# Optimization experiments

Measured on AMD Instinct MI355X. Metric: run time of the kernel, lower is better.

The kernel has to match this reference:

```python
import jax, jax.numpy as jnp
import numpy as np
import math

E = 8192        # number of hyperedges in the batch
IN_DIM = 256
OUT_DIM = 128


def setup_inputs() -> dict:
    key = jax.random.key(0)
    k1, k2, k3, k4 = jax.random.split(key, 4)
    node_embeddings = jax.random.normal(k1, (E, IN_DIM), dtype=jnp.float32)
    # xavier_uniform-like scale for the projection weights
    lim = 1.414 * math.sqrt(6.0 / (IN_DIM + OUT_DIM))
    query_weight = jax.random.uniform(k2, (IN_DIM, OUT_DIM), minval=-lim, maxval=lim, dtype=jnp.float32)
    key_weight = jax.random.uniform(k3, (IN_DIM, OUT_DIM), minval=-lim, maxval=lim, dtype=jnp.float32)
    # binary hypergraph connectivity mask [E, E]; diagonal forced to 1 so no row is fully masked
    mask = jax.random.randint(k4, (E, E), 0, 2, dtype=jnp.int32)
    mask = mask.at[jnp.arange(E), jnp.arange(E)].set(1)
    return {
        "node_embeddings": node_embeddings,
        "query_weight": query_weight,
        "key_weight": key_weight,
        "attention_mask": mask,
    }


def reference(node_embeddings, query_weight, key_weight, attention_mask):
    # QK projections: [E, in] x [in, out] -> [E, out]
    q = node_embeddings @ query_weight
    k = node_embeddings @ key_weight
    # scaled scores [E, E]
    scores = (q @ k.T) / jnp.sqrt(jnp.asarray(OUT_DIM, dtype=q.dtype))
    # masked_fill(mask == 0, -inf)
    scores = jnp.where(attention_mask == 0, jnp.asarray(-jnp.inf, dtype=scores.dtype), scores)
    probs = jax.nn.softmax(scores, axis=1)
    # output aggregates the KEY projections (as in the original code)
    return probs @ k
```

## Files before the change

### kernel.cpp

```cpp
#include <hip/hip_runtime.h>
#include <stdint.h>

#define E_N 8192
#define SPLIT 8
#define CH 16
#define QBLK 64

typedef unsigned short u16;
typedef unsigned int u32;
typedef unsigned long long u64;
typedef __attribute__((ext_vector_type(4))) float f32x4;
typedef __attribute__((ext_vector_type(8))) short bf16x8;
typedef __attribute__((ext_vector_type(4))) unsigned int u32x4;
typedef __attribute__((ext_vector_type(2))) unsigned int u32x2;

union V16 { u32x4 q; bf16x8 h; u16 u[8]; };

static __device__ __forceinline__ u16 f2bf(float f) {
  union { float f; unsigned u; } c; c.f = f;
  unsigned r = c.u + 0x7FFFu + ((c.u >> 16) & 1u);
  return (u16)(r >> 16);
}

constexpr float QS = 1.4426950408889634f / 11.313708498984761f;

__global__ void k_wt(const float* __restrict__ Wq, const float* __restrict__ Wk,
                     u16* __restrict__ wt) {
  int idx = blockIdx.x * 256 + threadIdx.x;
  int mat = idx >> 15, rem = idx & 32767;
  float v = mat ? Wk[rem] : Wq[rem];
  int d = rem >> 7, c = rem & 127;
  wt[(mat * 128 + c) * 256 + d] = f2bf(v);
}

__launch_bounds__(256)
__global__ void k_proj(const float* __restrict__ X, const u16* __restrict__ wt,
                       u16* __restrict__ qg, u16* __restrict__ kg) {
  __shared__ __align__(16) char Xs[64 * 512];
  const int tid = threadIdx.x;
  const int wid = tid >> 6, lane = tid & 63, g = lane >> 4, l15 = lane & 15;
  const int r0 = blockIdx.x * 64;
#pragma unroll
  for (int i = 0; i < 16; ++i) {
    int s = tid + 256 * i;
    int row = s >> 6, c4 = (s & 63) << 2;
    f32x4 v = *(const f32x4*)(X + (size_t)(r0 + row) * 256 + c4);
    u32x2 pk;
    pk[0] = f2bf(v[0]) | ((unsigned)f2bf(v[1]) << 16);
    pk[1] = f2bf(v[2]) | ((unsigned)f2bf(v[3]) << 16);
    *(u32x2*)(Xs + (((row << 9) + (c4 << 1)) ^ ((row & 7) << 4))) = pk;
  }
  __syncthreads();
  bf16x8 xa[8];
  const int arow = wid * 16 + l15;
#pragma unroll
  for (int ks = 0; ks < 8; ++ks) {
    V16 t; t.q = *(const u32x4*)(Xs + (((arow << 9) + (ks << 6) + (g << 4)) ^ ((l15 & 7) << 4)));
    xa[ks] = t.h;
  }
  const f32x4 zero4 = {0.f, 0.f, 0.f, 0.f};
  f32x4 acc[16];
#pragma unroll
  for (int i = 0; i < 16; ++i) acc[i] = zero4;
#pragma unroll
  for (int ct = 0; ct < 16; ++ct) {
    int mat = ct >> 3, c = ((ct & 7) << 4) + l15;
#pragma unroll
    for (int ks = 0; ks < 8; ++ks) {
      V16 b; b.q = *(const u32x4*)(wt + ((mat * 128 + c) * 256 + (ks << 5) + (g << 3)));
      acc[ct] = __builtin_amdgcn_mfma_f32_16x16x32_bf16(xa[ks], b.h, acc[ct], 0, 0, 0);
    }
  }
#pragma unroll
  for (int ct = 0; ct < 16; ++ct) {
    int mat = ct >> 3, c = ((ct & 7) << 4) + l15;
#pragma unroll
    for (int r = 0; r < 4; ++r) {
      int row = r0 + wid * 16 + 4 * g + r;
      float v = acc[ct][r];
      if (mat == 0) qg[row * 128 + c] = f2bf(v * QS);
      else          kg[row * 128 + c] = f2bf(v);
    }
  }
}

__global__ void k_kt(const u16* __restrict__ kg, u16* __restrict__ ktg) {
  __shared__ __align__(16) u16 Ts[64 * 66];
  const int tid = threadIdx.x;
  const int b = blockIdx.x;
  const int r0 = (b >> 1) * 64, c0 = (b & 1) * 64;
#pragma unroll
  for (int i = 0; i < 2; ++i) {
    int s = tid + 256 * i;
    int row = s >> 3, seg = s & 7;
    u32x4 v = *(const u32x4*)(kg + (size_t)(r0 + row) * 128 + c0 + seg * 8);
    unsigned* dst = (unsigned*)((char*)Ts + row * 132 + seg * 16);
    dst[0] = v[0]; dst[1] = v[1]; dst[2] = v[2]; dst[3] = v[3];
  }
  __syncthreads();
#pragma unroll
  for (int i = 0; i < 2; ++i) {
    int s = tid + 256 * i;
    int oc = s >> 3, seg2 = s & 7;
    u16 t[8];
#pragma unroll
    for (int j = 0; j < 8; ++j) t[j] = Ts[(seg2 * 8 + j) * 66 + oc];
    u32x4 o;
    o[0] = t[0] | ((unsigned)t[1] << 16);
    o[1] = t[2] | ((unsigned)t[3] << 16);
    o[2] = t[4] | ((unsigned)t[5] << 16);
    o[3] = t[6] | ((unsigned)t[7] << 16);
    *(u32x4*)(ktg + (size_t)(c0 + oc) * E_N + r0 + seg2 * 8) = o;
  }
}

#define LOADREGS(KV1)                                                           \
  {                                                                             \
    const u16* kp = kgp + (size_t)(KV1) * 128;                                  \
    kr0 = *(const u32x4*)(kp);                                                  \
    kr1 = *(const u32x4*)(kp + 16 * 128);                                       \
    kr2 = *(const u32x4*)(kp + 32 * 128);                                       \
    kr3 = *(const u32x4*)(kp + 48 * 128);                                       \
    const u16* tp = ktp + (KV1);                                                \
    tr0 = *(const u32x4*)(tp);                                                  \
    tr1 = *(const u32x4*)(tp + 32 * E_N);                                       \
    tr2 = *(const u32x4*)(tp + 64 * E_N);                                       \
    tr3 = *(const u32x4*)(tp + 96 * E_N);                                       \
  }

#define WRITELDS(KW, TW)                                                        \
  {                                                                             \
    *(u32x4*)((KW) + kofs)          = kr0;                                      \
    *(u32x4*)((KW) + kofs + 4096)   = kr1;                                      \
    *(u32x4*)((KW) + kofs + 8192)   = kr2;                                      \
    *(u32x4*)((KW) + kofs + 12288)  = kr3;                                      \
    *(u32x4*)((TW) + tofs)          = tr0;                                      \
    *(u32x4*)((TW) + tofs + 4096)   = tr1;                                      \
    *(u32x4*)((TW) + tofs + 8192)   = tr2;                                      \
    *(u32x4*)((TW) + tofs + 12288)  = tr3;                                      \
  }

#define MASKLOAD(KV1)                                                           \
  {                                                                             \
    _Pragma("unroll")                                                           \
    for (int j = 0; j < 16; ++j) mv[j] = mptr[(size_t)j * E_N + (KV1)];         \
  }

#define MASKBALLOT()                                                            \
  {                                                                             \
    u32 mlo = 0, mhi = 0;                                                       \
    _Pragma("unroll")                                                           \
    for (int j = 0; j < 16; ++j) {                                              \
      u64 b = __ballot(mv[j] != 0);                                             \
      if (lane == j) { mlo = (u32)b; mhi = (u32)(b >> 32); }                    \
    }                                                                           \
    if (lane < 16) { u32x2 o; o[0] = mlo; o[1] = mhi;                           \
      *(u32x2*)(MshW + lane * 2) = o; }                                         \
  }

#define FSTEP(SUB, KR, TR, KW, TW, DOPF)                                        \
  {                                                                             \
    if (DOPF) {                                                                 \
      LOADREGS(kvbase + (st2 + (SUB) + 1) * 64)                                 \
      MASKLOAD(kvbase + (st2 + (SUB) + 1) * 64)                                 \
    }                                                                           \
    u32 wlo[4], whi[4];                                                         \
    _Pragma("unroll")                                                           \
    for (int r = 0; r < 4; ++r) {                                               \
      u32x2 t3 = *(const u32x2*)(MshW + (4 * g + r) * 2);                       \
      wlo[r] = t3[0]; whi[r] = t3[1];                                           \
    }                                                                           \
    f32x4 S[4];                                                                 \
    _Pragma("unroll")                                                           \
    for (int t = 0; t < 4; ++t) S[t] = zero4;                                   \
    _Pragma("unroll")                                                           \
    for (int t = 0; t < 4; ++t) {                                               \
      int krow = t * 16 + l15;                                                  \
      _Pragma("unroll")                                                         \
      for (int ks = 0; ks < 4; ++ks) {                                          \
        V16 kf; kf.q = *(const u32x4*)((KR) + (((krow << 8) + (ks << 6) + (g << 4)) ^ ((l15 & 7) << 4))); \
        S[t] = __builtin_amdgcn_mfma_f32_16x16x32_bf16(qf[ks], kf.h, S[t], 0, 0, 0); \
      }                                                                         \
    }                                                                           \
    _Pragma("unroll")                                                           \
    for (int t = 0; t < 4; ++t) {                                               \
      _Pragma("unroll")                                                         \
      for (int r = 0; r < 4; ++r) {                                             \
        u32 w = (t & 2) ? whi[r] : wlo[r];                                      \
        float pv = ((w >> ((t & 1) * 16 + l15)) & 1u)                           \
                       ? __builtin_amdgcn_exp2f(S[t][r]) : 0.f;                 \
        lacc[r] += pv;                                                          \
        int prow = 4 * g + r;                                                   \
        *(u16*)(Pw + ((prow * 128 + (t * 16 + l15) * 2) ^ ((prow & 7) << 4))) = f2bf(pv); \
      }                                                                         \
    }                                                                           \
    bf16x8 pa0, pa1;                                                            \
    { V16 t2; t2.q = *(const u32x4*)(Pw + ((l15 * 128 + g * 16) ^ ((l15 & 7) << 4))); pa0 = t2.h; } \
    { V16 t2; t2.q = *(const u32x4*)(Pw + ((l15 * 128 + 64 + g * 16) ^ ((l15 & 7) << 4))); pa1 = t2.h; } \
    _Pragma("unroll")                                                           \
    for (int dt = 0; dt < 8; ++dt) {                                            \
      int krow = dt * 16 + l15;                                                 \
      V16 kf0; kf0.q = *(const u32x4*)((TR) + (((krow << 7) + (g << 4)) ^ ((l15 & 7) << 4))); \
      Oacc[dt] = __builtin_amdgcn_mfma_f32_16x16x32_bf16(pa0, kf0.h, Oacc[dt], 0, 0, 0); \
      V16 kf1; kf1.q = *(const u32x4*)((TR) + (((krow << 7) + 64 + (g << 4)) ^ ((l15 & 7) << 4))); \
      Oacc[dt] = __builtin_amdgcn_mfma_f32_16x16x32_bf16(pa1, kf1.h, Oacc[dt], 0, 0, 0); \
    }                                                                           \
    if (DOPF) MASKBALLOT()                                                      \
    __syncthreads();                                                            \
    if (DOPF) WRITELDS(KW, TW)                                                  \
    __syncthreads();                                                            \
  }

__launch_bounds__(256, 2)
__global__ void k_flash(const u16* __restrict__ qg, const u16* __restrict__ kg,
                        const u16* __restrict__ ktg, const int* __restrict__ M,
                        float* __restrict__ Op, float* __restrict__ lp) {
  __shared__ __align__(16) char K0[64 * 256], K1[64 * 256];
  __shared__ __align__(16) char T0[128 * 128], T1[128 * 128];
  __shared__ __align__(16) char Psh[4 * 2048];
  __shared__ __align__(8)  u32 Msh[4 * 32];
  const int tid = threadIdx.x;
  const int wid = tid >> 6, lane = tid & 63, g = lane >> 4, l15 = lane & 15;
  const int bid = blockIdx.x;
  const int split = bid & 7, qb = bid >> 3;
  const int qb0 = qb * QBLK;
  const int kvbase = split * (E_N / SPLIT);
  char* Pw = Psh + wid * 2048;
  u32* MshW = Msh + wid * 32;
  const int* mptr = M + (size_t)(qb0 + wid * 16) * E_N + lane;
  int mv[16];

  const int kr_r = tid >> 4, kr_s = tid & 15;
  const int tr_d = tid >> 3, tr_s = tid & 7;
  const int kofs = ((kr_r << 8) + (kr_s << 4)) ^ ((kr_r & 7) << 4);
  const int tofs = ((tr_d << 7) + (tr_s << 4)) ^ ((tr_d & 7) << 4);
  const u16* kgp = kg + (size_t)kr_r * 128 + kr_s * 8;
  const u16* ktp = ktg + (size_t)tr_d * E_N + tr_s * 8;
  u32x4 kr0, kr1, kr2, kr3, tr0, tr1, tr2, tr3;

  bf16x8 qf[4];
  {
    const u16* qrow = qg + (size_t)(qb0 + wid * 16 + l15) * 128;
#pragma unroll
    for (int ks = 0; ks < 4; ++ks) {
      V16 t; t.q = *(const u32x4*)(qrow + (ks << 5) + (g << 3));
      qf[ks] = t.h;
    }
  }
  const f32x4 zero4 = {0.f, 0.f, 0.f, 0.f};
  f32x4 Oacc[8];
#pragma unroll
  for (int i = 0; i < 8; ++i) Oacc[i] = zero4;
  float lacc[4] = {0.f, 0.f, 0.f, 0.f};

  MASKLOAD(kvbase)
  MASKBALLOT()
  LOADREGS(kvbase)
  WRITELDS(K0, T0)
  __syncthreads();

  for (int st2 = 0; st2 < CH; st2 += 2) {
    FSTEP(0, K0, T0, K1, T1, true)
    FSTEP(1, K1, T1, K0, T0, (st2 < CH - 2))
  }

#pragma unroll
  for (int r = 0; r < 4; ++r) {
    float v = lacc[r];
    v += __shfl_xor(v, 1);
    v += __shfl_xor(v, 2);
    v += __shfl_xor(v, 4);
    v += __shfl_xor(v, 8);
    lacc[r] = v;
  }
  if (l15 == 0) {
#pragma unroll
    for (int r = 0; r < 4; ++r)
      lp[split * E_N + qb0 + wid * 16 + 4 * g + r] = lacc[r];
  }
  float* op = Op + ((size_t)split * E_N + qb0 + wid * 16) * 128;
#pragma unroll
  for (int dt = 0; dt < 8; ++dt)
#pragma unroll
    for (int r = 0; r < 4; ++r)
      op[(4 * g + r) * 128 + dt * 16 + l15] = Oacc[dt][r];
}

__global__ void k_comb(const float* __restrict__ Op, const float* __restrict__ lp,
                       float* __restrict__ out) {
  int idx4 = blockIdx.x * 256 + threadIdx.x;
  int base = idx4 << 2;
  int e = base >> 7;
  f32x4 o = {0.f, 0.f, 0.f, 0.f};
  float l = 0.f;
#pragma unroll
  for (int s = 0; s < SPLIT; ++s) {
    o += *(const f32x4*)(Op + (size_t)s * (E_N * 128) + base);
    l += lp[s * E_N + e];
  }
  float rl = 1.0f / l;
  o[0] *= rl; o[1] *= rl; o[2] *= rl; o[3] *= rl;
  *(f32x4*)(out + base) = o;
}

extern "C" void kernel_launch(void* const* d_in, const int* in_sizes, int n_in,
                              void* d_out, int out_size, void* d_ws, size_t ws_size,
                              hipStream_t stream) {
  const float* X  = (const float*)d_in[0];
  const float* Wq = (const float*)d_in[1];
  const float* Wk = (const float*)d_in[2];
  const int*   M  = (const int*)d_in[3];
  char* ws = (char*)d_ws;
  u16*   qg   = (u16*)(ws);
  u16*   kg   = (u16*)(ws + (size_t)(2u << 20));
  u16*   ktg  = (u16*)(ws + (size_t)(4u << 20));
  u16*   wt   = (u16*)(ws + (size_t)(6u << 20));
  float* lp   = (float*)(ws + (size_t)(6u << 20) + (128u << 10));
  float* Op   = (float*)(ws + (size_t)(6u << 20) + (512u << 10) + (8u << 20));
  float* out = (float*)d_out;

  k_wt  <<<256, 256, 0, stream>>>(Wq, Wk, wt);
  k_proj<<<128, 256, 0, stream>>>(X, wt, qg, kg);
  k_kt  <<<256, 256, 0, stream>>>(kg, ktg);
  k_flash<<<SPLIT * (E_N / QBLK), 256, 0, stream>>>(qg, kg, ktg, M, Op, lp);
  k_comb<<<(E_N * 128 / 4) / 256, 256, 0, stream>>>(Op, lp, out);
}
```

Baseline: 134.6 us.

## Vectorize mask loads to 16-byte reads and stagger KV chunk order per block

```diff
diff --git a/kernel.cpp b/kernel.cpp
--- a/kernel.cpp
+++ b/kernel.cpp
@@ -143,16 +143,20 @@
 #define MASKLOAD(KV1)                                                           \
   {                                                                             \
     _Pragma("unroll")                                                           \
-    for (int j = 0; j < 16; ++j) mv[j] = mptr[(size_t)j * E_N + (KV1)];         \
+    for (int s = 0; s < 4; ++s)                                                 \
+      mq[s] = *(const u32x4*)(mbase + (size_t)(s * 4) * E_N + (KV1));           \
   }
 
 #define MASKBALLOT()                                                            \
   {                                                                             \
     u32 mlo = 0, mhi = 0;                                                       \
     _Pragma("unroll")                                                           \
-    for (int j = 0; j < 16; ++j) {                                              \
-      u64 b = __ballot(mv[j] != 0);                                             \
-      if (lane == j) { mlo = (u32)b; mhi = (u32)(b >> 32); }                    \
+    for (int s = 0; s < 4; ++s) {                                               \
+      _Pragma("unroll")                                                         \
+      for (int c = 0; c < 4; ++c) {                                             \
+        u64 b = __ballot(mq[s][c] != 0);                                        \
+        if (lane == s * 4 + c) { mlo = (u32)b; mhi = (u32)(b >> 32); }          \
+      }                                                                         \
     }                                                                           \
     if (lane < 16) { u32x2 o; o[0] = mlo; o[1] = mhi;                           \
       *(u32x2*)(MshW + lane * 2) = o; }                                         \
@@ -161,15 +165,13 @@
 #define FSTEP(SUB, KR, TR, KW, TW, DOPF)                                        \
   {                                                                             \
     if (DOPF) {                                                                 \
-      LOADREGS(kvbase + (st2 + (SUB) + 1) * 64)                                 \
-      MASKLOAD(kvbase + (st2 + (SUB) + 1) * 64)                                 \
-    }                                                                           \
-    u32 wlo[4], whi[4];                                                         \
-    _Pragma("unroll")                                                           \
-    for (int r = 0; r < 4; ++r) {                                               \
-      u32x2 t3 = *(const u32x2*)(MshW + (4 * g + r) * 2);                       \
-      wlo[r] = t3[0]; whi[r] = t3[1];                                           \
-    }                                                                           \
+      const int kvn = kvbase + (((st2 + (SUB) + 1 + qb) & 15) << 6);            \
+      LOADREGS(kvn)                                                             \
+      MASKLOAD(kvn)                                                             \
+    }                                                                           \
+    u32 wlo, whi;                                                               \
+    { u32x2 t3 = *(const u32x2*)(MshW + (g * 4 + (l15 & 3)) * 2);               \
+      wlo = t3[0]; whi = t3[1]; }                                               \
     f32x4 S[4];                                                                 \
     _Pragma("unroll")                                                           \
     for (int t = 0; t < 4; ++t) S[t] = zero4;                                   \
@@ -186,8 +188,8 @@
     for (int t = 0; t < 4; ++t) {                                               \
       _Pragma("unroll")                                                         \
       for (int r = 0; r < 4; ++r) {                                             \
-        u32 w = (t & 2) ? whi[r] : wlo[r];                                      \
-        float pv = ((w >> ((t & 1) * 16 + l15)) & 1u)                           \
+        u32 w = (r & 2) ? whi : wlo;                                            \
+        float pv = ((w >> ((r & 1) * 16 + t * 4 + q2)) & 1u)                    \
                        ? __builtin_amdgcn_exp2f(S[t][r]) : 0.f;                 \
         lacc[r] += pv;                                                          \
         int prow = 4 * g + r;                                                   \
@@ -221,14 +223,15 @@
   __shared__ __align__(8)  u32 Msh[4 * 32];
   const int tid = threadIdx.x;
   const int wid = tid >> 6, lane = tid & 63, g = lane >> 4, l15 = lane & 15;
+  const int q2 = l15 >> 2;
   const int bid = blockIdx.x;
   const int split = bid & 7, qb = bid >> 3;
   const int qb0 = qb * QBLK;
   const int kvbase = split * (E_N / SPLIT);
   char* Pw = Psh + wid * 2048;
   u32* MshW = Msh + wid * 32;
-  const int* mptr = M + (size_t)(qb0 + wid * 16) * E_N + lane;
-  int mv[16];
+  const int* mbase = M + (size_t)(qb0 + wid * 16 + (lane >> 4)) * E_N + 4 * (lane & 15);
+  u32x4 mq[4];
 
   const int kr_r = tid >> 4, kr_s = tid & 15;
   const int tr_d = tid >> 3, tr_s = tid & 7;
@@ -253,10 +256,13 @@
   for (int i = 0; i < 8; ++i) Oacc[i] = zero4;
   float lacc[4] = {0.f, 0.f, 0.f, 0.f};
 
-  MASKLOAD(kvbase)
-  MASKBALLOT()
-  LOADREGS(kvbase)
-  WRITELDS(K0, T0)
+  {
+    const int kv0 = kvbase + ((qb & 15) << 6);
+    MASKLOAD(kv0)
+    MASKBALLOT()
+    LOADREGS(kv0)
+    WRITELDS(K0, T0)
+  }
   __syncthreads();
 
   for (int st2 = 0; st2 < CH; st2 += 2) {
```

After: 135.1 us. No clear change (+0.4%).
